# Kernel tuning notes

Measured on AMD Instinct MI355X. Metric: run time of the kernel, lower is better.

Reference implementation:

```python
import jax, jax.numpy as jnp
import numpy as np

HOP = 768
NCB = 14
DIM = 512
VOCAB = 1024
W_SCALE = 0.02  # keep conv stacks numerically tame


def conv1d(x, w, b, stride=1, padding=0):
    # x: [B,C,L], w: [O,I,K] (torch layout), b: [O]
    y = jax.lax.conv_general_dilated(
        x, w, window_strides=(stride,), padding=[(padding, padding)],
        dimension_numbers=('NCH', 'OIH', 'NCH'))
    return y + b[None, :, None]


def conv_transpose1d(x, w, b, stride, padding):
    # torch ConvTranspose1d weight layout: (in, out, k)
    k = w.shape[2]
    w2 = jnp.flip(jnp.transpose(w, (1, 0, 2)), axis=2)  # -> OIH
    y = jax.lax.conv_general_dilated(
        x, w2, window_strides=(1,),
        padding=[(k - 1 - padding, k - 1 - padding)],
        lhs_dilation=(stride,),
        dimension_numbers=('NCH', 'OIH', 'NCH'))
    return y + b[None, :, None]


def setup_inputs() -> dict:
    key = jax.random.key(0)
    ks = jax.random.split(key, 16)
    f = lambda k, shp, s=W_SCALE: jax.random.normal(k, shp, dtype=jnp.float32) * s
    B, T = 2, 98304  # T = 768 * 128
    return {
        'audio': jax.random.normal(ks[0], (B, 1, T), dtype=jnp.float32),
        'codebooks': jax.random.normal(ks[1], (NCB, VOCAB, DIM), dtype=jnp.float32),
        'ew1': f(ks[2], (256, 1, 7)), 'eb1': f(ks[3], (256,)),
        'ew2': f(ks[4], (512, 256, 5)), 'eb2': f(ks[5], (512,)),
        'ew3': f(ks[6], (NCB * DIM, 512, 3)), 'eb3': f(ks[7], (NCB * DIM,)),
        'dw1': f(ks[8], (NCB * DIM, 512, 5)), 'db1': f(ks[9], (512,)),
        'dw2': f(ks[10], (256, 512, 5)), 'db2': f(ks[11], (256,)),
        'dw3': f(ks[12], (1, 256, 7)), 'db3': f(ks[13], (1,)),
    }


def reference(audio, codebooks, ew1, eb1, ew2, eb2, ew3, eb3,
              dw1, db1, dw2, db2, dw3, db3):
    B = audio.shape[0]
    # ---- encoder ----
    h = jax.nn.relu(conv1d(audio, ew1, eb1, stride=1, padding=3))
    h = jax.nn.relu(conv1d(h, ew2, eb2, stride=HOP, padding=2))
    h = conv1d(h, ew3, eb3, stride=1, padding=1)          # [B, NCB*DIM, S]
    S = h.shape[-1]
    emb = h.reshape(B, NCB, DIM, S).transpose(0, 1, 3, 2)  # [B, NCB, S, DIM]
    # ---- VQ: per-codebook squared L2 distance + argmin (same argmin as cdist) ----
    d2 = (jnp.sum(emb * emb, axis=-1, keepdims=True)            # [B,NCB,S,1]
          - 2.0 * jnp.einsum('bksd,kvd->bksv', emb, codebooks)  # [B,NCB,S,V]
          + jnp.sum(codebooks * codebooks, axis=-1)[None, :, None, :])
    codes = jnp.argmin(d2, axis=-1)                        # [B, NCB, S] int
    # ---- decode: embedding lookup + transposed conv decoder ----
    q = codebooks[jnp.arange(NCB)[None, :, None], codes]   # [B, NCB, S, DIM]
    q = q.transpose(0, 1, 3, 2).reshape(B, NCB * DIM, S)   # [B, NCB*DIM, S]
    a = jax.nn.relu(conv_transpose1d(q, dw1, db1, stride=HOP, padding=2))
    a = jax.nn.relu(conv1d(a, dw2, db2, stride=1, padding=2))
    a = jnp.tanh(conv1d(a, dw3, db3, stride=1, padding=3))
    return a  # [B, 1, (S-1)*HOP + 1]
```

## Files before the change

### kernel.cpp

```cpp
#include <hip/hip_runtime.h>
#include <hip/hip_bf16.h>
#include <math.h>

#define T_IN 98304
#define SS 128
#define NBATCH 2
#define NN 256
#define C1 256
#define C2 512
#define C3 7168
#define NCBK 14
#define DIMV 512
#define VOC 1024
#define TOUT 97537
#define HOP 768

#define OFF_CBN    0L
#define OFF_AB1    14336L
#define OFF_AB2    14848L
#define OFF_CCONST 15104L
#define OFF_H2C    15120L
#define OFF_H2XH   146192L
#define OFF_H2XL   342800L
#define OFF_H3H    539408L
#define OFF_H3L    1456912L
#define OFF_SCORES 2374416L
#define OFF_X1H    2374416L
#define OFF_X1L    2538256L
#define OFF_DW1T   539408L
#define OFF_XH     539408L
#define OFF_XL     3488528L
#define OFF_CODES  9714448L
#define OFF_QBF    9718032L
#define OFF_A1RAW  10635536L
#define OFF_A2ACT  11290896L

typedef __attribute__((ext_vector_type(8))) short short8;
typedef __attribute__((ext_vector_type(4))) float f32x4;

static __device__ inline ushort f2bf(float x) {
  __hip_bfloat16 h = __float2bfloat16(x);
  return *reinterpret_cast<ushort*>(&h);
}

static __device__ inline void split8(const float4 x0, const float4 x1,
                                     short8& h, short8& l) {
  float xs[8] = {x0.x, x0.y, x0.z, x0.w, x1.x, x1.y, x1.z, x1.w};
  #pragma unroll
  for (int e = 0; e < 8; ++e) {
    uint b = __float_as_uint(xs[e]);
    h[e] = (short)(b >> 16);
    float r = xs[e] - __uint_as_float(b & 0xffff0000u);
    l[e] = (short)(__float_as_uint(r) >> 16);
  }
}

__global__ void k_cbn(const float* __restrict__ cb, float* __restrict__ cbn) {
  int row = blockIdx.x * 4 + (threadIdx.x >> 6);
  int lane = threadIdx.x & 63;
  const float* p = cb + (long)row * DIMV;
  float s = 0.f;
  for (int d = lane; d < DIMV; d += 64) { float x = p[d]; s += x * x; }
  for (int off = 32; off; off >>= 1) s += __shfl_down(s, off);
  if (lane == 0) cbn[row] = s;
}

__global__ __launch_bounds__(256) void k_prep_ab2(const float* __restrict__ db1,
    const float* __restrict__ dw2, const float* __restrict__ db2,
    float* __restrict__ ab1, float* __restrict__ ab2) {
  __shared__ float red[256];
  int o = blockIdx.x, t = threadIdx.x;
  if (o == 0) { ab1[t] = fmaxf(db1[t], 0.f); ab1[t + 256] = fmaxf(db1[t + 256], 0.f); }
  const float* wp = dw2 + (long)o * C2 * 5;
  float acc = 0.f;
  #pragma unroll
  for (int h = 0; h < 2; ++h) {
    int c = t + h * 256;
    const float* p = wp + c * 5;
    float wsum = p[0] + p[1] + p[2] + p[3] + p[4];
    acc = fmaf(wsum, fmaxf(db1[c], 0.f), acc);
  }
  red[t] = acc;
  __syncthreads();
  for (int off = 128; off; off >>= 1) {
    if (t < off) red[t] += red[t + off];
    __syncthreads();
  }
  if (t == 0) ab2[o] = fmaxf(red[0] + db2[o], 0.f);
}

__global__ __launch_bounds__(256) void k_prep_c(const float* __restrict__ dw3,
    const float* __restrict__ db3, const float* __restrict__ ab2,
    float* __restrict__ cconst) {
  __shared__ float red[256];
  int t = threadIdx.x;
  float wsum3 = 0.f;
  #pragma unroll
  for (int j = 0; j < 7; ++j) wsum3 += dw3[t*7+j];
  red[t] = wsum3 * ab2[t];
  __syncthreads();
  for (int off = 128; off; off >>= 1) {
    if (t < off) red[t] += red[t + off];
    __syncthreads();
  }
  if (t == 0) cconst[0] = tanhf(red[0] + db3[0]);
}

__global__ __launch_bounds__(256) void k_enc1(const float* __restrict__ audio,
    const float* __restrict__ ew1, const float* __restrict__ eb1,
    ushort* __restrict__ X1h, ushort* __restrict__ X1l) {
  int n = blockIdx.x, ic = threadIdx.x;
  int b = n >> 7, s = n & 127;
  const float* ap = audio + (long)b * T_IN;
  int base = HOP * s - 5;
  float a[11];
  #pragma unroll
  for (int w = 0; w < 11; ++w) {
    int ai = base + w;
    a[w] = (ai >= 0 && ai < T_IN) ? ap[ai] : 0.f;
  }
  float w1[7];
  #pragma unroll
  for (int j = 0; j < 7; ++j) w1[j] = ew1[ic*7+j];
  float b1 = eb1[ic];
  long off = (long)n * 1280 + ic * 5;
  #pragma unroll
  for (int jj = 0; jj < 5; ++jj) {
    int tcol = HOP * s + jj - 2;
    float v = 0.f;
    if (tcol >= 0) {
      float acc = b1;
      #pragma unroll
      for (int j = 0; j < 7; ++j) acc = fmaf(w1[j], a[jj + j], acc);
      v = fmaxf(acc, 0.f);
    }
    uint bi = __float_as_uint(v);
    X1h[off + jj] = (ushort)(bi >> 16);
    float r = v - __uint_as_float(bi & 0xffff0000u);
    X1l[off + jj] = (ushort)(__float_as_uint(r) >> 16);
  }
}

__global__ __launch_bounds__(64) void gemm_enc2(const float* __restrict__ ew2,
    const ushort* __restrict__ X1h, const ushort* __restrict__ X1l,
    const float* __restrict__ eb2, float* __restrict__ h2c) {
  const int t = threadIdx.x;
  const int l15 = t & 15, quad = t >> 4;
  const int m0 = blockIdx.x * 32, n0 = blockIdx.y * 64;
  f32x4 acc[2][4] = {};
  const float*  aB = ew2 + (long)(m0 + l15) * 1280 + quad * 8;
  const ushort* bhB = X1h + (long)(n0 + l15) * 1280 + quad * 8;
  const ushort* blB = X1l + (long)(n0 + l15) * 1280 + quad * 8;
  for (int k0 = 0; k0 < 1280; k0 += 32) {
    short8 ah[2], al[2], bh[4], bl[4];
    #pragma unroll
    for (int f = 0; f < 2; ++f) {
      const float* ap = aB + (long)f * 16 * 1280 + k0;
      float4 x0 = *(const float4*)ap;
      float4 x1 = *(const float4*)(ap + 4);
      split8(x0, x1, ah[f], al[f]);
    }
    #pragma unroll
    for (int f = 0; f < 4; ++f) {
      bh[f] = *(const short8*)(bhB + (long)f * 16 * 1280 + k0);
      bl[f] = *(const short8*)(blB + (long)f * 16 * 1280 + k0);
    }
    #pragma unroll
    for (int i = 0; i < 2; ++i)
      #pragma unroll
      for (int j = 0; j < 4; ++j) {
        acc[i][j] = __builtin_amdgcn_mfma_f32_16x16x32_bf16(ah[i], bh[j], acc[i][j], 0, 0, 0);
        acc[i][j] = __builtin_amdgcn_mfma_f32_16x16x32_bf16(ah[i], bl[j], acc[i][j], 0, 0, 0);
        acc[i][j] = __builtin_amdgcn_mfma_f32_16x16x32_bf16(al[i], bh[j], acc[i][j], 0, 0, 0);
      }
  }
  #pragma unroll
  for (int i = 0; i < 2; ++i) {
    const int obase = m0 + i * 16 + quad * 4;
    float4 bias = *(const float4*)(eb2 + obase);
    #pragma unroll
    for (int j = 0; j < 4; ++j) {
      const int n = n0 + j * 16 + l15;
      float4 out;
      out.x = fmaxf(acc[i][j][0] + bias.x, 0.f);
      out.y = fmaxf(acc[i][j][1] + bias.y, 0.f);
      out.z = fmaxf(acc[i][j][2] + bias.z, 0.f);
      out.w = fmaxf(acc[i][j][3] + bias.w, 0.f);
      *(float4*)(h2c + (long)n * C2 + obase) = out;
    }
  }
}

__global__ void k_h2x(const float* __restrict__ h2c, ushort* __restrict__ h2xh,
                      ushort* __restrict__ h2xl) {
  int idx = blockIdx.x * 256 + threadIdx.x;
  const int total = NN * 1536;
  for (; idx < total; idx += gridDim.x * 256) {
    int n = idx / 1536, r = idx - n * 1536;
    int ic = r / 3, j = r - ic * 3;
    int s2 = (n & 127) + j - 1;
    int b = n >> 7;
    float v = (s2 >= 0 && s2 < SS) ? h2c[(long)(b*SS + s2)*C2 + ic] : 0.f;
    uint bi = __float_as_uint(v);
    h2xh[idx] = (ushort)(bi >> 16);
    float rr = v - __uint_as_float(bi & 0xffff0000u);
    h2xl[idx] = (ushort)(__float_as_uint(rr) >> 16);
  }
}

__global__ __launch_bounds__(256) void gemm_h3(const float* __restrict__ A,
    const ushort* __restrict__ Bh, const ushort* __restrict__ Bl,
    const float* __restrict__ eb3, ushort* __restrict__ h3h, ushort* __restrict__ h3l) {
  __shared__ __align__(16) float red[4 * 4096];
  const int tid = threadIdx.x;
  const int w = tid >> 6, lane = tid & 63;
  const int l15 = lane & 15, quad = lane >> 4;
  const int m0 = blockIdx.x * 64, n0 = blockIdx.y * 64;
  const int kbase = w * 384;
  f32x4 acc[4][4] = {};
  const float*  aB = A  + (long)(m0 + l15) * 1536 + kbase + quad * 8;
  const ushort* bhB = Bh + (long)(n0 + l15) * 1536 + kbase + quad * 8;
  const ushort* blB = Bl + (long)(n0 + l15) * 1536 + kbase + quad * 8;
  for (int k0 = 0; k0 < 384; k0 += 32) {
    short8 ah[4], al[4], bh[4], bl[4];
    #pragma unroll
    for (int f = 0; f < 4; ++f) {
      const float* ap = aB + (long)f * 16 * 1536 + k0;
      float4 x0 = *(const float4*)ap;
      float4 x1 = *(const float4*)(ap + 4);
      split8(x0, x1, ah[f], al[f]);
      bh[f] = *(const short8*)(bhB + (long)f * 16 * 1536 + k0);
      bl[f] = *(const short8*)(blB + (long)f * 16 * 1536 + k0);
    }
    #pragma unroll
    for (int i = 0; i < 4; ++i)
      #pragma unroll
      for (int j = 0; j < 4; ++j) {
        acc[i][j] = __builtin_amdgcn_mfma_f32_16x16x32_bf16(ah[i], bh[j], acc[i][j], 0, 0, 0);
        acc[i][j] = __builtin_amdgcn_mfma_f32_16x16x32_bf16(ah[i], bl[j], acc[i][j], 0, 0, 0);
        acc[i][j] = __builtin_amdgcn_mfma_f32_16x16x32_bf16(al[i], bh[j], acc[i][j], 0, 0, 0);
      }
  }
  #pragma unroll
  for (int i = 0; i < 4; ++i)
    #pragma unroll
    for (int j = 0; j < 4; ++j)
      *(float4*)&red[w * 4096 + (i * 4 + j) * 256 + lane * 4] = *(float4*)&acc[i][j];
  __syncthreads();
  const int mbase = m0 + w * 16 + quad * 4;
  float4 bias = *(const float4*)(eb3 + mbase);
  #pragma unroll
  for (int j = 0; j < 4; ++j) {
    float4 s = *(const float4*)&red[(w * 4 + j) * 256 + lane * 4];
    #pragma unroll
    for (int r = 1; r < 4; ++r) {
      float4 tt = *(const float4*)&red[r * 4096 + (w * 4 + j) * 256 + lane * 4];
      s.x += tt.x; s.y += tt.y; s.z += tt.z; s.w += tt.w;
    }
    const int n = n0 + j * 16 + l15;
    float v0 = s.x + bias.x;
    float v1 = s.y + bias.y;
    float v2 = s.z + bias.z;
    float v3 = s.w + bias.w;
    uint b0 = __float_as_uint(v0), b1 = __float_as_uint(v1);
    uint b2 = __float_as_uint(v2), b3 = __float_as_uint(v3);
    uint2 hp;
    hp.x = (b0 >> 16) | (b1 & 0xffff0000u);
    hp.y = (b2 >> 16) | (b3 & 0xffff0000u);
    float r0 = v0 - __uint_as_float(b0 & 0xffff0000u);
    float r1 = v1 - __uint_as_float(b1 & 0xffff0000u);
    float r2 = v2 - __uint_as_float(b2 & 0xffff0000u);
    float r3 = v3 - __uint_as_float(b3 & 0xffff0000u);
    uint2 lp;
    lp.x = (__float_as_uint(r0) >> 16) | (__float_as_uint(r1) & 0xffff0000u);
    lp.y = (__float_as_uint(r2) >> 16) | (__float_as_uint(r3) & 0xffff0000u);
    long off = (long)n * C3 + mbase;
    *(uint2*)(h3h + off) = hp;
    *(uint2*)(h3l + off) = lp;
  }
}

__global__ __launch_bounds__(256) void gemm_scores(const float* __restrict__ cb,
    const ushort* __restrict__ h3h, const ushort* __restrict__ h3l,
    const float* __restrict__ cbn, float* __restrict__ scores) {
  __shared__ __align__(16) float red[4 * 4096];
  const int tid = threadIdx.x;
  const int w = tid >> 6, lane = tid & 63;
  const int l15 = lane & 15, quad = lane >> 4;
  const int m0 = blockIdx.x * 64, n0 = blockIdx.y * 64, z = blockIdx.z;
  const int kbase = w * 128;
  f32x4 acc[4][4] = {};
  const float*  aB = cb + (long)z * VOC * DIMV + (long)(m0 + l15) * 512 + kbase + quad * 8;
  const ushort* bhB = h3h + (long)(n0 + l15) * C3 + z * 512 + kbase + quad * 8;
  const ushort* blB = h3l + (long)(n0 + l15) * C3 + z * 512 + kbase + quad * 8;
  for (int k0 = 0; k0 < 128; k0 += 32) {
    short8 ah[4], al[4], bh[4], bl[4];
    #pragma unroll
    for (int f = 0; f < 4; ++f) {
      const float* ap = aB + (long)f * 16 * 512 + k0;
      float4 x0 = *(const float4*)ap;
      float4 x1 = *(const float4*)(ap + 4);
      split8(x0, x1, ah[f], al[f]);
      bh[f] = *(const short8*)(bhB + (long)f * 16 * C3 + k0);
      bl[f] = *(const short8*)(blB + (long)f * 16 * C3 + k0);
    }
    #pragma unroll
    for (int i = 0; i < 4; ++i)
      #pragma unroll
      for (int j = 0; j < 4; ++j) {
        acc[i][j] = __builtin_amdgcn_mfma_f32_16x16x32_bf16(ah[i], bh[j], acc[i][j], 0, 0, 0);
        acc[i][j] = __builtin_amdgcn_mfma_f32_16x16x32_bf16(ah[i], bl[j], acc[i][j], 0, 0, 0);
        acc[i][j] = __builtin_amdgcn_mfma_f32_16x16x32_bf16(al[i], bh[j], acc[i][j], 0, 0, 0);
      }
  }
  #pragma unroll
  for (int i = 0; i < 4; ++i)
    #pragma unroll
    for (int j = 0; j < 4; ++j)
      *(float4*)&red[w * 4096 + (i * 4 + j) * 256 + lane * 4] = *(float4*)&acc[i][j];
  __syncthreads();
  const int vbase = m0 + w * 16 + quad * 4;
  float4 cn = *(const float4*)(cbn + z * VOC + vbase);
  #pragma unroll
  for (int j = 0; j < 4; ++j) {
    float4 s = *(const float4*)&red[(w * 4 + j) * 256 + lane * 4];
    #pragma unroll
    for (int r = 1; r < 4; ++r) {
      float4 tt = *(const float4*)&red[r * 4096 + (w * 4 + j) * 256 + lane * 4];
      s.x += tt.x; s.y += tt.y; s.z += tt.z; s.w += tt.w;
    }
    const int n = n0 + j * 16 + l15;
    float4 out;
    out.x = cn.x - 2.f * s.x;
    out.y = cn.y - 2.f * s.y;
    out.z = cn.z - 2.f * s.z;
    out.w = cn.w - 2.f * s.w;
    *(float4*)(scores + ((long)z * NN + n) * VOC + vbase) = out;
  }
}

__global__ void k_argmin(const float* __restrict__ scores, int* __restrict__ codes) {
  int row = blockIdx.x;
  int lane = threadIdx.x;
  const float* p = scores + (long)row * VOC;
  float best = 3.4e38f; int bi = 0;
  for (int i = 0; i < 16; ++i) {
    int v = i * 64 + lane;
    float x = p[v];
    if (x < best) { best = x; bi = v; }
  }
  for (int off = 32; off; off >>= 1) {
    float ob = __shfl_down(best, off);
    int oi = __shfl_down(bi, off);
    if (ob < best || (ob == best && oi < bi)) { best = ob; bi = oi; }
  }
  if (lane == 0) codes[row] = bi;
}

__global__ __launch_bounds__(256) void k_dw1t(const float* __restrict__ dw1,
                                              ushort* __restrict__ dw1t) {
  __shared__ __align__(16) ushort T[64 * 72];
  int t = threadIdx.x;
  int k0 = blockIdx.x * 64, m0 = blockIdx.y * 64;
  int kk = t >> 2, mj = (t & 3) * 16;
  const float* src = dw1 + (long)(k0 + kk) * 2560 + m0 + mj;
  float x[16];
  *(float4*)&x[0]  = *(const float4*)(src);
  *(float4*)&x[4]  = *(const float4*)(src + 4);
  *(float4*)&x[8]  = *(const float4*)(src + 8);
  *(float4*)&x[12] = *(const float4*)(src + 12);
  #pragma unroll
  for (int l = 0; l < 16; ++l)
    T[(mj + l) * 72 + kk] = f2bf(x[l]);
  __syncthreads();
  int mo = t >> 2, kc = (t & 3) * 16;
  uint4 u0 = *(const uint4*)&T[mo * 72 + kc];
  uint4 u1 = *(const uint4*)&T[mo * 72 + kc + 8];
  ushort* dst = dw1t + (long)(m0 + mo) * C3 + k0 + kc;
  *(uint4*)dst = u0;
  *(uint4*)(dst + 8) = u1;
}

__global__ void k_gather_qbf(const float* __restrict__ cb, const int* __restrict__ codes,
                             ushort* __restrict__ qbf) {
  int idx = blockIdx.x * 256 + threadIdx.x;
  const int total = NN * C3 / 2;
  if (idx >= total) return;
  int n = idx / 3584, rr = idx - n * 3584;
  int k = rr >> 8, dp = rr & 255;
  int code = codes[k * NN + n];
  const float* s = cb + ((long)(k * VOC + code)) * DIMV + dp * 2;
  uint lo = f2bf(s[0]), hi = f2bf(s[1]);
  ((uint*)qbf)[idx] = lo | (hi << 16);
}

__global__ __launch_bounds__(256) void gemm_a1_mfma(const ushort* __restrict__ dw1t,
    const ushort* __restrict__ qbf, float* __restrict__ a1raw) {
  __shared__ __align__(16) float red[4 * 4096];
  const int tid = threadIdx.x;
  const int w = tid >> 6, lane = tid & 63;
  const int l15 = lane & 15, quad = lane >> 4;
  const int m0 = blockIdx.x * 64, n0 = blockIdx.y * 64;
  const int kbase = w * 1792;
  f32x4 acc[4][4] = {};
  const ushort* aB = dw1t + (long)(m0 + l15) * C3 + kbase + quad * 8;
  const ushort* bB = qbf  + (long)(n0 + l15) * C3 + kbase + quad * 8;
  #pragma unroll 2
  for (int k0 = 0; k0 < 1792; k0 += 32) {
    short8 ah[4], bh[4];
    #pragma unroll
    for (int f = 0; f < 4; ++f) {
      ah[f] = *(const short8*)(aB + (long)f * 16 * C3 + k0);
      bh[f] = *(const short8*)(bB + (long)f * 16 * C3 + k0);
    }
    #pragma unroll
    for (int i = 0; i < 4; ++i)
      #pragma unroll
      for (int j = 0; j < 4; ++j)
        acc[i][j] = __builtin_amdgcn_mfma_f32_16x16x32_bf16(ah[i], bh[j], acc[i][j], 0, 0, 0);
  }
  #pragma unroll
  for (int i = 0; i < 4; ++i)
    #pragma unroll
    for (int j = 0; j < 4; ++j)
      *(float4*)&red[w * 4096 + (i * 4 + j) * 256 + lane * 4] = *(float4*)&acc[i][j];
  __syncthreads();
  #pragma unroll
  for (int j = 0; j < 4; ++j) {
    float4 s = *(const float4*)&red[(w * 4 + j) * 256 + lane * 4];
    #pragma unroll
    for (int r = 1; r < 4; ++r) {
      float4 tt = *(const float4*)&red[r * 4096 + (w * 4 + j) * 256 + lane * 4];
      s.x += tt.x; s.y += tt.y; s.z += tt.z; s.w += tt.w;
    }
    const int n = n0 + j * 16 + l15;
    const int mb = m0 + w * 16 + quad * 4;
    float v[4] = {s.x, s.y, s.z, s.w};
    #pragma unroll
    for (int reg = 0; reg < 4; ++reg) {
      int m = mb + reg;
      int c = m / 5, jj = m - c * 5;
      a1raw[((long)(n * 5 + jj)) * C2 + c] = v[reg];
    }
  }
}

__global__ void k_x2(const float* __restrict__ a1raw, const float* __restrict__ ab1g,
                     const float* __restrict__ db1, ushort* __restrict__ Xh,
                     ushort* __restrict__ Xl) {
  int idx = blockIdx.x * 256 + threadIdx.x;
  const int total = 2304 * 2560;
  for (; idx < total; idx += gridDim.x * 256) {
    int nu = idx / 2560, ck = idx - nu * 2560;
    int n = nu / 9, u = nu - n * 9;
    int c = ck / 5, jj = ck - c * 5;
    int w = u + jj;
    int s = n & 127;
    int tc = HOP * s - 6 + w;
    float v;
    if (tc < 0 || tc > TOUT - 1) v = 0.f;
    else if (w >= 4 && w <= 8)
      v = fmaxf(db1[c] + a1raw[((long)(n * 5 + (w - 4))) * C2 + c], 0.f);
    else v = ab1g[c];
    uint bi = __float_as_uint(v);
    Xh[idx] = (ushort)(bi >> 16);
    float rr = v - __uint_as_float(bi & 0xffff0000u);
    Xl[idx] = (ushort)(__float_as_uint(rr) >> 16);
  }
}

__global__ __launch_bounds__(256) void gemm_dec2(const float* __restrict__ dw2,
    const ushort* __restrict__ Xh, const ushort* __restrict__ Xl,
    const float* __restrict__ db2, float* __restrict__ a2act) {
  __shared__ __align__(16) float red[4 * 4096];
  const int tid = threadIdx.x;
  const int w = tid >> 6, lane = tid & 63;
  const int l15 = lane & 15, quad = lane >> 4;
  const int m0 = blockIdx.x * 64, n0 = blockIdx.y * 64;
  const int kbase = w * 640;
  f32x4 acc[4][4] = {};
  const float*  aB = dw2 + (long)(m0 + l15) * 2560 + kbase + quad * 8;
  const ushort* bhB = Xh + (long)(n0 + l15) * 2560 + kbase + quad * 8;
  const ushort* blB = Xl + (long)(n0 + l15) * 2560 + kbase + quad * 8;
  for (int k0 = 0; k0 < 640; k0 += 32) {
    short8 ah[4], al[4], bh[4], bl[4];
    #pragma unroll
    for (int f = 0; f < 4; ++f) {
      const float* ap = aB + (long)f * 16 * 2560 + k0;
      float4 x0 = *(const float4*)ap;
      float4 x1 = *(const float4*)(ap + 4);
      split8(x0, x1, ah[f], al[f]);
      bh[f] = *(const short8*)(bhB + (long)f * 16 * 2560 + k0);
      bl[f] = *(const short8*)(blB + (long)f * 16 * 2560 + k0);
    }
    #pragma unroll
    for (int i = 0; i < 4; ++i)
      #pragma unroll
      for (int j = 0; j < 4; ++j) {
        acc[i][j] = __builtin_amdgcn_mfma_f32_16x16x32_bf16(ah[i], bh[j], acc[i][j], 0, 0, 0);
        acc[i][j] = __builtin_amdgcn_mfma_f32_16x16x32_bf16(ah[i], bl[j], acc[i][j], 0, 0, 0);
        acc[i][j] = __builtin_amdgcn_mfma_f32_16x16x32_bf16(al[i], bh[j], acc[i][j], 0, 0, 0);
      }
  }
  #pragma unroll
  for (int i = 0; i < 4; ++i)
    #pragma unroll
    for (int j = 0; j < 4; ++j)
      *(float4*)&red[w * 4096 + (i * 4 + j) * 256 + lane * 4] = *(float4*)&acc[i][j];
  __syncthreads();
  const int mb = m0 + w * 16 + quad * 4;
  float4 bias = *(const float4*)(db2 + mb);
  #pragma unroll
  for (int j = 0; j < 4; ++j) {
    float4 s = *(const float4*)&red[(w * 4 + j) * 256 + lane * 4];
    #pragma unroll
    for (int r = 1; r < 4; ++r) {
      float4 tt = *(const float4*)&red[r * 4096 + (w * 4 + j) * 256 + lane * 4];
      s.x += tt.x; s.y += tt.y; s.z += tt.z; s.w += tt.w;
    }
    const int nu = n0 + j * 16 + l15;
    float4 out;
    out.x = fmaxf(s.x + bias.x, 0.f);
    out.y = fmaxf(s.y + bias.y, 0.f);
    out.z = fmaxf(s.z + bias.z, 0.f);
    out.w = fmaxf(s.w + bias.w, 0.f);
    *(float4*)(a2act + (long)nu * C1 + mb) = out;
  }
}

__global__ void k_fill(float* __restrict__ outp, const float* __restrict__ cconst) {
  float v = cconst[0];
  int idx = blockIdx.x * 256 + threadIdx.x;
  const int total = NBATCH * TOUT;
  for (; idx < total; idx += gridDim.x * 256) outp[idx] = v;
}

__global__ __launch_bounds__(256) void k_dec3(const float* __restrict__ a2act,
    const float* __restrict__ ab2g, const float* __restrict__ dw3,
    const float* __restrict__ db3, float* __restrict__ outp) {
  __shared__ float sa2[9 * C1];
  __shared__ float sb[C1];
  int n = blockIdx.x;
  int s = n & 127, b = n >> 7;
  int t = threadIdx.x;
  for (int i = t; i < 9 * C1; i += 256) sa2[i] = a2act[(long)n * 9 * C1 + i];
  sb[t] = ab2g[t];
  __syncthreads();
  int wv = t >> 6, lane = t & 63;
  float b3 = db3[0];
  for (int w15 = wv; w15 < 15; w15 += 4) {
    int tc = HOP * s - 7 + w15;
    if (tc < 0 || tc > TOUT - 1) continue;
    float part = 0.f;
    for (int cc = lane; cc < C1; cc += 64) {
      #pragma unroll
      for (int j = 0; j < 7; ++j) {
        int wcol = tc + j - 3;
        float x;
        if (wcol < 0 || wcol > TOUT - 1) x = 0.f;
        else {
          int du = wcol - (HOP * s - 4);
          x = (du >= 0 && du <= 8) ? sa2[du * C1 + cc] : sb[cc];
        }
        part = fmaf(dw3[cc*7+j], x, part);
      }
    }
    for (int off = 32; off; off >>= 1) part += __shfl_down(part, off);
    if (lane == 0) outp[(long)b * TOUT + tc] = tanhf(part + b3);
  }
}

extern "C" void kernel_launch(void* const* d_in, const int* in_sizes, int n_in,
                              void* d_out, int out_size, void* d_ws, size_t ws_size,
                              hipStream_t stream) {
  const float* audio = (const float*)d_in[0];
  const float* cb    = (const float*)d_in[1];
  const float* ew1   = (const float*)d_in[2];
  const float* eb1   = (const float*)d_in[3];
  const float* ew2   = (const float*)d_in[4];
  const float* eb2   = (const float*)d_in[5];
  const float* ew3   = (const float*)d_in[6];
  const float* eb3   = (const float*)d_in[7];
  const float* dw1   = (const float*)d_in[8];
  const float* db1   = (const float*)d_in[9];
  const float* dw2   = (const float*)d_in[10];
  const float* db2   = (const float*)d_in[11];
  const float* dw3   = (const float*)d_in[12];
  const float* db3   = (const float*)d_in[13];
  float* outp = (float*)d_out;
  float* ws = (float*)d_ws;

  float*  cbn    = ws + OFF_CBN;
  float*  ab1    = ws + OFF_AB1;
  float*  ab2    = ws + OFF_AB2;
  float*  cconst = ws + OFF_CCONST;
  float*  h2c    = ws + OFF_H2C;
  ushort* h2xh   = (ushort*)(ws + OFF_H2XH);
  ushort* h2xl   = (ushort*)(ws + OFF_H2XL);
  ushort* h3h    = (ushort*)(ws + OFF_H3H);
  ushort* h3l    = (ushort*)(ws + OFF_H3L);
  float*  scores = ws + OFF_SCORES;
  ushort* X1h    = (ushort*)(ws + OFF_X1H);
  ushort* X1l    = (ushort*)(ws + OFF_X1L);
  ushort* dw1t   = (ushort*)(ws + OFF_DW1T);
  ushort* Xh     = (ushort*)(ws + OFF_XH);
  ushort* Xl     = (ushort*)(ws + OFF_XL);
  int*    codes  = (int*)(ws + OFF_CODES);
  ushort* qbf    = (ushort*)(ws + OFF_QBF);
  float*  a1raw  = ws + OFF_A1RAW;
  float*  a2act  = ws + OFF_A2ACT;

  k_cbn<<<3584, 256, 0, stream>>>(cb, cbn);
  k_prep_ab2<<<C1, 256, 0, stream>>>(db1, dw2, db2, ab1, ab2);
  k_prep_c<<<1, 256, 0, stream>>>(dw3, db3, ab2, cconst);
  k_enc1<<<NN, 256, 0, stream>>>(audio, ew1, eb1, X1h, X1l);
  gemm_enc2<<<dim3(16, 4), 64, 0, stream>>>(ew2, X1h, X1l, eb2, h2c);
  k_h2x<<<384, 256, 0, stream>>>(h2c, h2xh, h2xl);
  gemm_h3<<<dim3(112, 4), 256, 0, stream>>>(ew3, h2xh, h2xl, eb3, h3h, h3l);
  gemm_scores<<<dim3(16, 4, 14), 256, 0, stream>>>(cb, h3h, h3l, cbn, scores);
  k_argmin<<<NCBK * NN, 64, 0, stream>>>(scores, codes);
  k_dw1t<<<dim3(112, 40), 256, 0, stream>>>(dw1, dw1t);
  k_gather_qbf<<<3584, 256, 0, stream>>>(cb, codes, qbf);
  gemm_a1_mfma<<<dim3(40, 4), 256, 0, stream>>>(dw1t, qbf, a1raw);
  k_x2<<<4096, 256, 0, stream>>>(a1raw, ab1, db1, Xh, Xl);
  gemm_dec2<<<dim3(4, 36), 256, 0, stream>>>(dw2, Xh, Xl, db2, a2act);
  k_fill<<<256, 256, 0, stream>>>(outp, cconst);
  k_dec3<<<NN, 256, 0, stream>>>(a2act, ab2, dw3, db3, outp);
}
```

Measured before the change: 465.0 us.

## Split K across more waves in enc2 and a1 GEMMs with LDS reduction

```diff
diff --git a/kernel.cpp b/kernel.cpp
--- a/kernel.cpp
+++ b/kernel.cpp
@@ -141,17 +141,20 @@
   }
 }
 
-__global__ __launch_bounds__(64) void gemm_enc2(const float* __restrict__ ew2,
+__global__ __launch_bounds__(256) void gemm_enc2(const float* __restrict__ ew2,
     const ushort* __restrict__ X1h, const ushort* __restrict__ X1l,
     const float* __restrict__ eb2, float* __restrict__ h2c) {
-  const int t = threadIdx.x;
-  const int l15 = t & 15, quad = t >> 4;
+  __shared__ __align__(16) float red[4 * 2048];
+  const int tid = threadIdx.x;
+  const int w = tid >> 6, lane = tid & 63;
+  const int l15 = lane & 15, quad = lane >> 4;
   const int m0 = blockIdx.x * 32, n0 = blockIdx.y * 64;
+  const int kbase = w * 320;
   f32x4 acc[2][4] = {};
-  const float*  aB = ew2 + (long)(m0 + l15) * 1280 + quad * 8;
-  const ushort* bhB = X1h + (long)(n0 + l15) * 1280 + quad * 8;
-  const ushort* blB = X1l + (long)(n0 + l15) * 1280 + quad * 8;
-  for (int k0 = 0; k0 < 1280; k0 += 32) {
+  const float*  aB = ew2 + (long)(m0 + l15) * 1280 + kbase + quad * 8;
+  const ushort* bhB = X1h + (long)(n0 + l15) * 1280 + kbase + quad * 8;
+  const ushort* blB = X1l + (long)(n0 + l15) * 1280 + kbase + quad * 8;
+  for (int k0 = 0; k0 < 320; k0 += 32) {
     short8 ah[2], al[2], bh[4], bl[4];
     #pragma unroll
     for (int f = 0; f < 2; ++f) {
@@ -175,19 +178,30 @@
       }
   }
   #pragma unroll
-  for (int i = 0; i < 2; ++i) {
+  for (int i = 0; i < 2; ++i)
+    #pragma unroll
+    for (int j = 0; j < 4; ++j)
+      *(float4*)&red[w * 2048 + (i * 4 + j) * 256 + lane * 4] = *(float4*)&acc[i][j];
+  __syncthreads();
+  #pragma unroll
+  for (int q = 0; q < 2; ++q) {
+    const int c = 2 * w + q;
+    const int i = c >> 2, j = c & 3;
+    float4 s = make_float4(0.f, 0.f, 0.f, 0.f);
+    #pragma unroll
+    for (int g = 0; g < 4; ++g) {
+      float4 t4 = *(const float4*)&red[g * 2048 + c * 256 + lane * 4];
+      s.x += t4.x; s.y += t4.y; s.z += t4.z; s.w += t4.w;
+    }
     const int obase = m0 + i * 16 + quad * 4;
     float4 bias = *(const float4*)(eb2 + obase);
-    #pragma unroll
-    for (int j = 0; j < 4; ++j) {
-      const int n = n0 + j * 16 + l15;
-      float4 out;
-      out.x = fmaxf(acc[i][j][0] + bias.x, 0.f);
-      out.y = fmaxf(acc[i][j][1] + bias.y, 0.f);
-      out.z = fmaxf(acc[i][j][2] + bias.z, 0.f);
-      out.w = fmaxf(acc[i][j][3] + bias.w, 0.f);
-      *(float4*)(h2c + (long)n * C2 + obase) = out;
-    }
+    const int n = n0 + j * 16 + l15;
+    float4 out;
+    out.x = fmaxf(s.x + bias.x, 0.f);
+    out.y = fmaxf(s.y + bias.y, 0.f);
+    out.z = fmaxf(s.z + bias.z, 0.f);
+    out.w = fmaxf(s.w + bias.w, 0.f);
+    *(float4*)(h2c + (long)n * C2 + obase) = out;
   }
 }
 
@@ -394,19 +408,19 @@
   ((uint*)qbf)[idx] = lo | (hi << 16);
 }
 
-__global__ __launch_bounds__(256) void gemm_a1_mfma(const ushort* __restrict__ dw1t,
+__global__ __launch_bounds__(1024) void gemm_a1_mfma(const ushort* __restrict__ dw1t,
     const ushort* __restrict__ qbf, float* __restrict__ a1raw) {
   __shared__ __align__(16) float red[4 * 4096];
   const int tid = threadIdx.x;
   const int w = tid >> 6, lane = tid & 63;
   const int l15 = lane & 15, quad = lane >> 4;
   const int m0 = blockIdx.x * 64, n0 = blockIdx.y * 64;
-  const int kbase = w * 1792;
+  const int kbase = w * 448;
   f32x4 acc[4][4] = {};
   const ushort* aB = dw1t + (long)(m0 + l15) * C3 + kbase + quad * 8;
   const ushort* bB = qbf  + (long)(n0 + l15) * C3 + kbase + quad * 8;
   #pragma unroll 2
-  for (int k0 = 0; k0 < 1792; k0 += 32) {
+  for (int k0 = 0; k0 < 448; k0 += 32) {
     short8 ah[4], bh[4];
     #pragma unroll
     for (int f = 0; f < 4; ++f) {
@@ -419,29 +433,33 @@
       for (int j = 0; j < 4; ++j)
         acc[i][j] = __builtin_amdgcn_mfma_f32_16x16x32_bf16(ah[i], bh[j], acc[i][j], 0, 0, 0);
   }
-  #pragma unroll
-  for (int i = 0; i < 4; ++i)
-    #pragma unroll
-    for (int j = 0; j < 4; ++j)
-      *(float4*)&red[w * 4096 + (i * 4 + j) * 256 + lane * 4] = *(float4*)&acc[i][j];
-  __syncthreads();
-  #pragma unroll
-  for (int j = 0; j < 4; ++j) {
-    float4 s = *(const float4*)&red[(w * 4 + j) * 256 + lane * 4];
-    #pragma unroll
-    for (int r = 1; r < 4; ++r) {
-      float4 tt = *(const float4*)&red[r * 4096 + (w * 4 + j) * 256 + lane * 4];
-      s.x += tt.x; s.y += tt.y; s.z += tt.z; s.w += tt.w;
-    }
-    const int n = n0 + j * 16 + l15;
-    const int mb = m0 + w * 16 + quad * 4;
-    float v[4] = {s.x, s.y, s.z, s.w};
-    #pragma unroll
-    for (int reg = 0; reg < 4; ++reg) {
-      int m = mb + reg;
-      int c = m / 5, jj = m - c * 5;
-      a1raw[((long)(n * 5 + jj)) * C2 + c] = v[reg];
-    }
+  float4 rsum = make_float4(0.f, 0.f, 0.f, 0.f);
+  #pragma unroll
+  for (int r = 0; r < 4; ++r) {
+    if ((w >> 2) == r) {
+      #pragma unroll
+      for (int i = 0; i < 4; ++i)
+        #pragma unroll
+        for (int j = 0; j < 4; ++j)
+          *(float4*)&red[(w & 3) * 4096 + (i * 4 + j) * 256 + lane * 4] = *(float4*)&acc[i][j];
+    }
+    __syncthreads();
+    #pragma unroll
+    for (int g = 0; g < 4; ++g) {
+      float4 t4 = *(const float4*)&red[g * 4096 + w * 256 + lane * 4];
+      rsum.x += t4.x; rsum.y += t4.y; rsum.z += t4.z; rsum.w += t4.w;
+    }
+    __syncthreads();
+  }
+  const int ci = w >> 2, cj = w & 3;
+  const int n = n0 + cj * 16 + l15;
+  const int mb = m0 + ci * 16 + quad * 4;
+  float v[4] = {rsum.x, rsum.y, rsum.z, rsum.w};
+  #pragma unroll
+  for (int reg = 0; reg < 4; ++reg) {
+    int m = mb + reg;
+    int c = m / 5, jj = m - c * 5;
+    a1raw[((long)(n * 5 + jj)) * C2 + c] = v[reg];
   }
 }
 
@@ -614,14 +632,14 @@
   k_prep_ab2<<<C1, 256, 0, stream>>>(db1, dw2, db2, ab1, ab2);
   k_prep_c<<<1, 256, 0, stream>>>(dw3, db3, ab2, cconst);
   k_enc1<<<NN, 256, 0, stream>>>(audio, ew1, eb1, X1h, X1l);
-  gemm_enc2<<<dim3(16, 4), 64, 0, stream>>>(ew2, X1h, X1l, eb2, h2c);
+  gemm_enc2<<<dim3(16, 4), 256, 0, stream>>>(ew2, X1h, X1l, eb2, h2c);
   k_h2x<<<384, 256, 0, stream>>>(h2c, h2xh, h2xl);
   gemm_h3<<<dim3(112, 4), 256, 0, stream>>>(ew3, h2xh, h2xl, eb3, h3h, h3l);
   gemm_scores<<<dim3(16, 4, 14), 256, 0, stream>>>(cb, h3h, h3l, cbn, scores);
   k_argmin<<<NCBK * NN, 64, 0, stream>>>(scores, codes);
   k_dw1t<<<dim3(112, 40), 256, 0, stream>>>(dw1, dw1t);
   k_gather_qbf<<<3584, 256, 0, stream>>>(cb, codes, qbf);
-  gemm_a1_mfma<<<dim3(40, 4), 256, 0, stream>>>(dw1t, qbf, a1raw);
+  gemm_a1_mfma<<<dim3(40, 4), 1024, 0, stream>>>(dw1t, qbf, a1raw);
   k_x2<<<4096, 256, 0, stream>>>(a1raw, ab1, db1, Xh, Xl);
   gemm_dec2<<<dim3(4, 36), 256, 0, stream>>>(dw2, Xh, Xl, db2, a2act);
   k_fill<<<256, 256, 0, stream>>>(outp, cconst);
```

Result: faster. 441.9 us (-5.0%).
